# Kernel tuning notes

Hardware: AMD Instinct MI355X
Metric: run time of the kernel (lower is better)

## Reference

```python
import math
import jax, jax.numpy as jnp
import numpy as np

B, S, D, H, DH, R, V = 8, 1024, 1024, 8, 512, 36, 32002  # DH = d_model//2, HD = h*DH = 4096
HD = H * DH
LN_EPS = 1e-5


def setup_inputs() -> dict:
    key = jax.random.key(0)
    ks = jax.random.split(key, 16)

    def n(k, shp, std=0.02):
        return jax.random.normal(k, shp, jnp.float32) * std

    pre_words = jax.random.randint(ks[0], (B, S), 0, V)
    img_features = jax.random.normal(ks[1], (B, R, D), jnp.float32)
    exp_embed = n(ks[2], (V, D)).at[0].set(0.0)  # padding_idx=0
    # id2visual table: sparse nonneg rows over 36 regions; zero rows -> textual tokens
    id2vis = (jax.random.uniform(ks[3], (V, R)) < 0.05).astype(jnp.float32)
    # stacked params for 2 transformer layers; weights stored (in, out) so y = x @ W + b
    wq = n(ks[4], (2, D, HD)); bq = jnp.zeros((2, HD), jnp.float32)
    wk = n(ks[5], (2, D, HD)); bk = jnp.zeros((2, HD), jnp.float32)
    wv = n(ks[6], (2, D, HD)); bv = jnp.zeros((2, HD), jnp.float32)
    wo = n(ks[7], (2, HD, D)); bo = jnp.zeros((2, D), jnp.float32)
    w1 = n(ks[8], (2, D, D)); b1 = jnp.zeros((2, D), jnp.float32)
    w2 = n(ks[9], (2, D, D)); b2 = jnp.zeros((2, D), jnp.float32)
    ln1_g = jnp.ones((2, D), jnp.float32); ln1_b = jnp.zeros((2, D), jnp.float32)
    ln2_g = jnp.ones((2, D), jnp.float32); ln2_b = jnp.zeros((2, D), jnp.float32)
    return dict(pre_words=pre_words, img_features=img_features, exp_embed=exp_embed,
                id2vis=id2vis, wq=wq, bq=bq, wk=wk, bk=bk, wv=wv, bv=bv, wo=wo, bo=bo,
                w1=w1, b1=b1, w2=w2, b2=b2, ln1_g=ln1_g, ln1_b=ln1_b, ln2_g=ln2_g, ln2_b=ln2_b)


def _layer_norm(x, g, b):
    m = x.mean(-1, keepdims=True)
    v = ((x - m) ** 2).mean(-1, keepdims=True)
    return (x - m) / jnp.sqrt(v + LN_EPS) * g + b


def _softmax_one(x):
    # shifted-denominator softmax: exp(x - max) / (1 + sum exp(x - max))
    x = x - x.max(-1, keepdims=True)
    e = jnp.exp(x)
    return e / (1.0 + e.sum(-1, keepdims=True))


def reference(pre_words, img_features, exp_embed, id2vis, wq, bq, wk, bk, wv, bv,
              wo, bo, w1, b1, w2, b2, ln1_g, ln1_b, ln2_g, ln2_b):
    # token embedding: textual (masked to 0 where a visual row exists) + visual bmm
    te = exp_embed[pre_words]                       # (B,S,D)
    vids = id2vis[pre_words]                        # (B,S,R)
    word_mask = vids.sum(-1, keepdims=True) != 0    # (B,S,1)
    ve = jnp.einsum('bsr,brd->bsd', vids, img_features)
    x = jnp.where(word_mask, 0.0, te) + ve          # (B,S,D)

    scale = 1.0 / math.sqrt(DH)
    for i in range(2):  # two structurally identical transformer layers
        h = _layer_norm(x, ln1_g[i], ln1_b[i])
        q = (h @ wq[i] + bq[i]).reshape(B, S, H, DH).transpose(0, 2, 1, 3)
        k = (h @ wk[i] + bk[i]).reshape(B, S, H, DH).transpose(0, 2, 1, 3)
        v = (h @ wv[i] + bv[i]).reshape(B, S, H, DH).transpose(0, 2, 1, 3)
        attn = _softmax_one(jnp.einsum('bhqd,bhkd->bhqk', q, k) * scale)  # (B,H,S,S)
        o = jnp.einsum('bhqk,bhkd->bhqd', attn, v)
        o = o.transpose(0, 2, 1, 3).reshape(B, S, HD)
        x = x + (o @ wo[i] + bo[i])
        f = _layer_norm(x, ln2_g[i], ln2_b[i])
        f = jax.nn.gelu(f @ w1[i] + b1[i], approximate=False) @ w2[i] + b2[i]
        x = x + f
    return x
```

## Files before the change

### kernel.cpp

```cpp
#include <hip/hip_runtime.h>


using u16 = unsigned short;
typedef __attribute__((ext_vector_type(8))) short bf16x8;
typedef __attribute__((ext_vector_type(4))) float f32x4;

__device__ __forceinline__ float b2f(u16 u) {
  union { unsigned int i; float f; } v; v.i = ((unsigned int)u) << 16; return v.f;
}
__device__ __forceinline__ u16 f2b(float f) {
  union { float f; unsigned int i; } v; v.f = f;
  unsigned int i = v.i;
  return (u16)((i + 0x7FFFu + ((i >> 16) & 1u)) >> 16);
}
__device__ __forceinline__ float gelu_f(float x) {
  return 0.5f * x * (1.f + erff(x * 0.70710678118654752f));
}
__device__ __forceinline__ void async16(void* lds, const void* g) {
  __builtin_amdgcn_global_load_lds((const __attribute__((address_space(1))) void*)g,
                                   (__attribute__((address_space(3))) void*)lds, 16, 0, 0);
}
__device__ __forceinline__ void storeC(float* p, float v) { *p = v; }
__device__ __forceinline__ void storeC(u16* p, float v) { *p = f2b(v); }

__global__ __launch_bounds__(256) void embed_k(
    const int* __restrict__ words, const float* __restrict__ img,
    const float* __restrict__ emb, const float* __restrict__ id2v,
    float* __restrict__ x)
{
  __shared__ float vs[36];
  int tok = blockIdx.x, b = tok >> 10, t = threadIdx.x;
  int wd = words[tok];
  if (t < 36) vs[t] = id2v[(size_t)wd * 36 + t];
  __syncthreads();
  bool any = false;
#pragma unroll
  for (int r = 0; r < 36; ++r) any = any || (vs[r] != 0.f);
#pragma unroll
  for (int i = 0; i < 4; ++i) {
    int d = t + (i << 8);
    float acc = 0.f;
    for (int r = 0; r < 36; ++r) {
      float vv = vs[r];
      if (vv != 0.f) acc += vv * img[((size_t)(b * 36 + r) << 10) + d];
    }
    float te = any ? 0.f : emb[((size_t)wd << 10) + d];
    x[((size_t)tok << 10) + d] = te + acc;
  }
}

__global__ __launch_bounds__(256) void ln_k(
    const float* __restrict__ x, u16* __restrict__ out,
    const float* __restrict__ g, const float* __restrict__ bb)
{
  __shared__ float red[4];
  int row = blockIdx.x, t = threadIdx.x;
  const float* xr = x + ((size_t)row << 10);
  float v[4], s = 0.f;
#pragma unroll
  for (int i = 0; i < 4; ++i) { v[i] = xr[t + (i << 8)]; s += v[i]; }
#pragma unroll
  for (int o = 32; o; o >>= 1) s += __shfl_xor(s, o, 64);
  if ((t & 63) == 0) red[t >> 6] = s;
  __syncthreads();
  s = red[0] + red[1] + red[2] + red[3];
  float mean = s * 0.0009765625f;
  float q = 0.f;
#pragma unroll
  for (int i = 0; i < 4; ++i) { float d = v[i] - mean; q += d * d; }
  __syncthreads();
#pragma unroll
  for (int o = 32; o; o >>= 1) q += __shfl_xor(q, o, 64);
  if ((t & 63) == 0) red[t >> 6] = q;
  __syncthreads();
  q = red[0] + red[1] + red[2] + red[3];
  float rstd = rsqrtf(q * 0.0009765625f + 1e-5f);
  u16* orow = out + ((size_t)row << 10);
#pragma unroll
  for (int i = 0; i < 4; ++i) {
    int d = t + (i << 8);
    orow[d] = f2b((v[i] - mean) * rstd * g[d] + bb[d]);
  }
}

__global__ __launch_bounds__(256) void sm_k(const u16* __restrict__ S, u16* __restrict__ P)
{
  __shared__ float red[4];
  size_t row = blockIdx.x;
  int t = threadIdx.x;
  const u16* sr = S + (row << 10);
  ushort4 sv = *(const ushort4*)(sr + (t << 2));
  float v[4] = { b2f(sv.x), b2f(sv.y), b2f(sv.z), b2f(sv.w) };
  float m = fmaxf(fmaxf(v[0], v[1]), fmaxf(v[2], v[3]));
#pragma unroll
  for (int o = 32; o; o >>= 1) m = fmaxf(m, __shfl_xor(m, o, 64));
  if ((t & 63) == 0) red[t >> 6] = m;
  __syncthreads();
  m = fmaxf(fmaxf(red[0], red[1]), fmaxf(red[2], red[3]));
  float e[4], s = 0.f;
#pragma unroll
  for (int i = 0; i < 4; ++i) { e[i] = __expf(v[i] - m); s += e[i]; }
  __syncthreads();
#pragma unroll
  for (int o = 32; o; o >>= 1) s += __shfl_xor(s, o, 64);
  if ((t & 63) == 0) red[t >> 6] = s;
  __syncthreads();
  s = red[0] + red[1] + red[2] + red[3];
  float inv = 1.f / (1.f + s);
  ushort4 pv;
  pv.x = f2b(e[0] * inv); pv.y = f2b(e[1] * inv);
  pv.z = f2b(e[2] * inv); pv.w = f2b(e[3] * inv);
  *(ushort4*)(P + (row << 10) + (t << 2)) = pv;
}

__global__ __launch_bounds__(256) void tr_k(
    const float* __restrict__ src, u16* __restrict__ dst, int ls, int ld)
{
  __shared__ u16 tile[64][65];
  int c0 = blockIdx.x << 6, r0 = blockIdx.y << 6;
  int tx = threadIdx.x & 63, ty0 = threadIdx.x >> 6;
#pragma unroll
  for (int i = 0; i < 16; ++i) {
    int ty = (ty0 << 4) + i;
    tile[ty][tx] = f2b(src[(size_t)(r0 + ty) * ls + (c0 + tx)]);
  }
  __syncthreads();
#pragma unroll
  for (int i = 0; i < 16; ++i) {
    int ty = (ty0 << 4) + i;
    dst[(size_t)(c0 + ty) * ld + (r0 + tx)] = tile[tx][ty];
  }
}

template <typename CT, int ACT, int BIAS, int RESID>
__global__ __launch_bounds__(512, 1) void gemm8p(
    const u16* __restrict__ A, const u16* __restrict__ Bt,
    CT* __restrict__ C, const float* __restrict__ bias,
    const float* __restrict__ resid,
    int M, int N, int K, int lda, int ldb, int ldc, float scale,
    int zbase, int zdiv, int ga, int gb, int gc,
    long long aS1, long long aS2, long long bS1, long long bS2,
    long long cS1, long long cS2)
{
  __shared__ u16 lA[2][256 * 64];
  __shared__ u16 lB[2][256 * 64];
  const int nwg = gridDim.x * gridDim.y;
  const int id = blockIdx.y * gridDim.x + blockIdx.x;
  const int qq = nwg >> 3, rr8 = nwg & 7;
  const int xcd = id & 7, off = id >> 3;
  const int swz = (xcd < rr8 ? xcd * (qq + 1) : rr8 * (qq + 1) + (xcd - rr8) * qq) + off;
  const int bx = swz % gridDim.x, by = swz / gridDim.x;

  long long lz = blockIdx.z;
  long long gz = zbase + lz;
  long long zA = ga ? gz : lz, zB = gb ? gz : lz, zC = gc ? gz : lz;
  size_t aOff = (size_t)((zA / zdiv) * aS1 + (zA % zdiv) * aS2);
  size_t bOff = (size_t)((zB / zdiv) * bS1 + (zB % zdiv) * bS2);
  size_t cOff = (size_t)((zC / zdiv) * cS1 + (zC % zdiv) * cS2);
  const int m0 = by << 8, n0 = bx << 8;
  const int tid = threadIdx.x, lane = tid & 63, w = tid >> 6;
  const int wm = w >> 2, wn = w & 3;
  const int srow8 = lane >> 3;
  const int schunk = (lane & 7) ^ srow8;
  const int fr = lane & 15, hi = lane >> 4;

  f32x4 acc[8][4];
#pragma unroll
  for (int mi = 0; mi < 8; ++mi)
#pragma unroll
    for (int ni = 0; ni < 4; ++ni) acc[mi][ni] = 0.f;

  const u16* Ab = A + aOff;
  const u16* Bb = Bt + bOff;

  auto ST_B = [&](int buf, int k0) {
#pragma unroll
    for (int s = 0; s < 4; ++s) {
      const int rb = (s << 6) + (w << 3);
      async16(&lB[buf][rb << 6], Bb + (size_t)(n0 + rb + srow8) * ldb + (k0 + (schunk << 3)));
    }
  };
  auto ST_A02 = [&](int buf, int k0) {
#pragma unroll
    for (int s = 0; s < 4; s += 2) {
      const int rb = (s << 6) + (w << 3);
      async16(&lA[buf][rb << 6], Ab + (size_t)(m0 + rb + srow8) * lda + (k0 + (schunk << 3)));
    }
  };
  auto ST_A13 = [&](int buf, int k0) {
#pragma unroll
    for (int s = 1; s < 4; s += 2) {
      const int rb = (s << 6) + (w << 3);
      async16(&lA[buf][rb << 6], Ab + (size_t)(m0 + rb + srow8) * lda + (k0 + (schunk << 3)));
    }
  };

  const int nt = K >> 6;
  ST_B(0, 0); ST_A02(0, 0); ST_A13(0, 0);
  ST_B(1, 64); ST_A02(1, 64);

  for (int t = 0; t < nt; ++t) {
    const int cur = t & 1;
    if (t + 1 < nt) asm volatile("s_waitcnt vmcnt(6)" ::: "memory");
    else            asm volatile("s_waitcnt vmcnt(0)" ::: "memory");
    __builtin_amdgcn_s_barrier();
    __builtin_amdgcn_sched_barrier(0);

    bf16x8 b8[4][2];
    const int kt2 = (t + 2) << 6;
#pragma unroll
    for (int p = 0; p < 4; ++p) {
      if (p == 0) {
#pragma unroll
        for (int ni = 0; ni < 4; ++ni)
#pragma unroll
          for (int ks = 0; ks < 2; ++ks) {
            const int R = (wn << 6) + (ni << 4) + fr;
            const int q = (ks << 2) + hi;
            b8[ni][ks] = *(const bf16x8*)&lB[cur][(R << 6) + ((q ^ (R & 7)) << 3)];
          }
      }
      bf16x8 a8[2][2];
#pragma unroll
      for (int i = 0; i < 2; ++i)
#pragma unroll
        for (int ks = 0; ks < 2; ++ks) {
          const int mi = (p << 1) + i;
          const int R = (wm << 7) + (mi << 4) + fr;
          const int q = (ks << 2) + hi;
          a8[i][ks] = *(const bf16x8*)&lA[cur][(R << 6) + ((q ^ (R & 7)) << 3)];
        }
      if (p == 0) { if (t + 1 < nt) ST_A13(cur ^ 1, (t + 1) << 6); }
      else if (p == 1) { if (t + 2 < nt) ST_B(cur, kt2); }
      else if (p == 2) { if (t + 2 < nt) ST_A02(cur, kt2); }
      __builtin_amdgcn_s_barrier();
      asm volatile("s_waitcnt lgkmcnt(0)" ::: "memory");
      __builtin_amdgcn_sched_barrier(0);
      __builtin_amdgcn_s_setprio(1);
#pragma unroll
      for (int i = 0; i < 2; ++i)
#pragma unroll
        for (int ni = 0; ni < 4; ++ni)
#pragma unroll
          for (int ks = 0; ks < 2; ++ks)
            acc[(p << 1) + i][ni] =
                __builtin_amdgcn_mfma_f32_16x16x32_bf16(a8[i][ks], b8[ni][ks],
                                                        acc[(p << 1) + i][ni], 0, 0, 0);
      __builtin_amdgcn_s_setprio(0);
      __builtin_amdgcn_s_barrier();
      __builtin_amdgcn_sched_barrier(0);
    }
  }

  const int r4 = hi << 2, cc = fr;
#pragma unroll
  for (int mi = 0; mi < 8; ++mi) {
#pragma unroll
    for (int ni = 0; ni < 4; ++ni) {
      const int col = n0 + (wn << 6) + (ni << 4) + cc;
      float bcol = 0.f;
      if (BIAS == 1) bcol = bias[col];
#pragma unroll
      for (int j = 0; j < 4; ++j) {
        const int row = m0 + (wm << 7) + (mi << 4) + r4 + j;
        float v = acc[mi][ni][j] * scale + bcol;
        if (BIAS == 2) v += bias[row];
        if (ACT == 1) v = gelu_f(v);
        const size_t idx = cOff + (size_t)row * ldc + col;
        if (RESID) v += resid[idx];
        storeC(&C[idx], v);
      }
    }
  }
}

template <typename CT, int ACT, int BIAS, int RESID, int BN>
__global__ __launch_bounds__(256, 4) void gemm_t(
    const u16* __restrict__ A, const u16* __restrict__ Bt,
    CT* __restrict__ C, const float* __restrict__ bias,
    const float* __restrict__ resid,
    int M, int N, int K, int lda, int ldb, int ldc, float scale,
    int zbase, int zdiv, int ga, int gb, int gc,
    long long aS1, long long aS2, long long bS1, long long bS2,
    long long cS1, long long cS2)
{
  constexpr int NACC = BN / 32;
  __shared__ u16 lA[128 * 64];
  __shared__ u16 lB[BN * 64];
  const int nwg = gridDim.x * gridDim.y;
  const int id = blockIdx.y * gridDim.x + blockIdx.x;
  const int qq = nwg >> 3, rr8 = nwg & 7;
  const int xcd = id & 7, off = id >> 3;
  const int swz = (xcd < rr8 ? xcd * (qq + 1) : rr8 * (qq + 1) + (xcd - rr8) * qq) + off;
  const int bx = swz % gridDim.x, by = swz / gridDim.x;

  long long lz = blockIdx.z;
  long long gz = zbase + lz;
  long long zA = ga ? gz : lz, zB = gb ? gz : lz, zC = gc ? gz : lz;
  size_t aOff = (size_t)((zA / zdiv) * aS1 + (zA % zdiv) * aS2);
  size_t bOff = (size_t)((zB / zdiv) * bS1 + (zB % zdiv) * bS2);
  size_t cOff = (size_t)((zC / zdiv) * cS1 + (zC % zdiv) * cS2);
  const int m0 = by << 7, n0 = bx * BN;
  const int tid = threadIdx.x, lane = tid & 63, w = tid >> 6;
  const int wm = w >> 1, wn = w & 1;
  const int srow8 = lane >> 3;
  const int schunk = (lane & 7) ^ srow8;
  const int fr = lane & 15, hi = lane >> 4;

  f32x4 acc[4][NACC];
#pragma unroll
  for (int mi = 0; mi < 4; ++mi)
#pragma unroll
    for (int ni = 0; ni < NACC; ++ni) acc[mi][ni] = 0.f;

  const u16* Ab = A + aOff;
  const u16* Bb = Bt + bOff;

  for (int k0 = 0; k0 < K; k0 += 64) {
#pragma unroll
    for (int s = 0; s < 4; ++s) {
      const int rb = (s << 5) + (w << 3);
      async16(&lA[rb << 6], Ab + (size_t)(m0 + rb + srow8) * lda + (k0 + (schunk << 3)));
    }
#pragma unroll
    for (int s = 0; s < BN / 32; ++s) {
      const int rb = (s << 5) + (w << 3);
      async16(&lB[rb << 6], Bb + (size_t)(n0 + rb + srow8) * ldb + (k0 + (schunk << 3)));
    }
    __syncthreads();
#pragma unroll
    for (int ks = 0; ks < 2; ++ks) {
      const int q = (ks << 2) + hi;
      bf16x8 a8[4], b8[NACC];
#pragma unroll
      for (int mi = 0; mi < 4; ++mi) {
        const int R = (wm << 6) + (mi << 4) + fr;
        a8[mi] = *(const bf16x8*)&lA[(R << 6) + ((q ^ (R & 7)) << 3)];
      }
#pragma unroll
      for (int ni = 0; ni < NACC; ++ni) {
        const int R = wn * (BN / 2) + (ni << 4) + fr;
        b8[ni] = *(const bf16x8*)&lB[(R << 6) + ((q ^ (R & 7)) << 3)];
      }
#pragma unroll
      for (int mi = 0; mi < 4; ++mi)
#pragma unroll
        for (int ni = 0; ni < NACC; ++ni)
          acc[mi][ni] = __builtin_amdgcn_mfma_f32_16x16x32_bf16(a8[mi], b8[ni], acc[mi][ni], 0, 0, 0);
    }
    __syncthreads();
  }

  const int r4 = hi << 2, cc = fr;
#pragma unroll
  for (int mi = 0; mi < 4; ++mi) {
#pragma unroll
    for (int ni = 0; ni < NACC; ++ni) {
      const int col = n0 + wn * (BN / 2) + (ni << 4) + cc;
      float bcol = 0.f;
      if (BIAS == 1) bcol = bias[col];
#pragma unroll
      for (int j = 0; j < 4; ++j) {
        const int row = m0 + (wm << 6) + (mi << 4) + r4 + j;
        float v = acc[mi][ni][j] * scale + bcol;
        if (BIAS == 2) v += bias[row];
        if (ACT == 1) v = gelu_f(v);
        const size_t idx = cOff + (size_t)row * ldc + col;
        if (RESID) v += resid[idx];
        storeC(&C[idx], v);
      }
    }
  }
}

extern "C" void kernel_launch(void* const* d_in, const int* in_sizes, int n_in,
                              void* d_out, int out_size, void* d_ws, size_t ws_size,
                              hipStream_t stream)
{
  (void)in_sizes; (void)n_in; (void)out_size;
  const int*   pre_words = (const int*)d_in[0];
  const float* img  = (const float*)d_in[1];
  const float* emb  = (const float*)d_in[2];
  const float* id2v = (const float*)d_in[3];
  const float* wq = (const float*)d_in[4];  const float* bq = (const float*)d_in[5];
  const float* wk = (const float*)d_in[6];  const float* bk = (const float*)d_in[7];
  const float* wv = (const float*)d_in[8];  const float* bv = (const float*)d_in[9];
  const float* wo = (const float*)d_in[10]; const float* bo = (const float*)d_in[11];
  const float* w1 = (const float*)d_in[12]; const float* b1 = (const float*)d_in[13];
  const float* w2 = (const float*)d_in[14]; const float* b2 = (const float*)d_in[15];
  const float* ln1g = (const float*)d_in[16]; const float* ln1b = (const float*)d_in[17];
  const float* ln2g = (const float*)d_in[18]; const float* ln2b = (const float*)d_in[19];

  const size_t FIXED = 88080384 + (size_t)(1 << 16);
  int g = 1;
  for (int c = 8; c >= 1; c >>= 1)
    if (FIXED + (size_t)c * 33554432 + 4194304 <= ws_size) { g = c; break; }
  int nc = 1;
  int ncmax = 8 * g > 32 ? 32 : 8 * g;
  for (int c = ncmax; c >= 1; c >>= 1)
    if (FIXED + (size_t)g * 33554432 + (size_t)c * 4194304 <= ws_size) { nc = c; break; }

  char* p = (char*)d_ws;
  auto alloc = [&](size_t bytes) -> void* {
    void* r = (void*)p; p += (bytes + 255) & ~(size_t)255; return r;
  };
  float* x  = (float*)alloc((size_t)8192 * 1024 * 4);
  u16* h    = (u16*)alloc((size_t)8192 * 1024 * 2);
  u16* Qg   = (u16*)alloc((size_t)g * 1024 * 4096 * 2);
  u16* Og   = (u16*)alloc((size_t)g * 1024 * 4096 * 2);
  u16* ff   = Qg;
  u16* Kg   = (u16*)alloc((size_t)g * 1024 * 4096 * 2);
  u16* Vtg  = (u16*)alloc((size_t)g * 4096 * 1024 * 2);
  u16* wqt  = (u16*)alloc((size_t)4096 * 1024 * 2);
  u16* wkt  = (u16*)alloc((size_t)4096 * 1024 * 2);
  u16* wvt  = (u16*)alloc((size_t)4096 * 1024 * 2);
  u16* wot  = (u16*)alloc((size_t)1024 * 4096 * 2);
  u16* w1t  = (u16*)alloc((size_t)1024 * 1024 * 2);
  u16* w2t  = (u16*)alloc((size_t)1024 * 1024 * 2);
  u16* Sc   = (u16*)alloc((size_t)nc << 21);
  u16* Pp   = (u16*)alloc((size_t)nc << 21);

  embed_k<<<8192, 256, 0, stream>>>(pre_words, img, emb, id2v, x);

  const float qk_scale = 0.044194173824159216f;
  for (int L = 0; L < 2; ++L) {
    const float* WQ = wq + (size_t)L * 1024 * 4096;
    const float* WK = wk + (size_t)L * 1024 * 4096;
    const float* WV = wv + (size_t)L * 1024 * 4096;
    const float* WO = wo + (size_t)L * 4096 * 1024;
    const float* W1 = w1 + (size_t)L * 1024 * 1024;
    const float* W2 = w2 + (size_t)L * 1024 * 1024;

    tr_k<<<dim3(64, 16), 256, 0, stream>>>(WQ, wqt, 4096, 1024);
    tr_k<<<dim3(64, 16), 256, 0, stream>>>(WK, wkt, 4096, 1024);
    tr_k<<<dim3(64, 16), 256, 0, stream>>>(WV, wvt, 4096, 1024);
    tr_k<<<dim3(16, 64), 256, 0, stream>>>(WO, wot, 1024, 4096);
    tr_k<<<dim3(16, 16), 256, 0, stream>>>(W1, w1t, 1024, 1024);
    tr_k<<<dim3(16, 16), 256, 0, stream>>>(W2, w2t, 1024, 1024);

    ln_k<<<8192, 256, 0, stream>>>(x, h, ln1g + L * 1024, ln1b + L * 1024);

    for (int g0 = 0; g0 < 8; g0 += g) {
      const u16* hg = h + (size_t)g0 * 1048576;
      const int Mg = 1024 * g;
      gemm8p<u16, 0, 1, 0><<<dim3(16, Mg >> 8), 512, 0, stream>>>(
          hg, wqt, Qg, bq + (size_t)L * 4096, nullptr,
          Mg, 4096, 1024, 1024, 1024, 4096, 1.f,
          0, 1, 0, 0, 0, 0, 0, 0, 0, 0, 0);
      gemm8p<u16, 0, 1, 0><<<dim3(16, Mg >> 8), 512, 0, stream>>>(
          hg, wkt, Kg, bk + (size_t)L * 4096, nullptr,
          Mg, 4096, 1024, 1024, 1024, 4096, 1.f,
          0, 1, 0, 0, 0, 0, 0, 0, 0, 0, 0);
      gemm8p<u16, 0, 2, 0><<<dim3(4, 16, g), 512, 0, stream>>>(
          wvt, h, Vtg, bv + (size_t)L * 4096, nullptr,
          4096, 1024, 1024, 1024, 1024, 1024, 1.f,
          g0, 1, 0, 1, 0, 0, 0, 1048576LL, 0, 4194304LL, 0);
      for (int c0 = 0; c0 < 8 * g; c0 += nc) {
        gemm8p<u16, 0, 0, 0><<<dim3(4, 4, nc), 512, 0, stream>>>(
            Qg, Kg, Sc, nullptr, nullptr,
            1024, 1024, 512, 4096, 4096, 1024, qk_scale,
            c0, 8, 1, 1, 0,
            4194304LL, 512LL, 4194304LL, 512LL, 8388608LL, 1048576LL);
        sm_k<<<nc << 10, 256, 0, stream>>>(Sc, Pp);
        gemm8p<u16, 0, 0, 0><<<dim3(2, 4, nc), 512, 0, stream>>>(
            Pp, Vtg, Og, nullptr, nullptr,
            1024, 512, 1024, 1024, 1024, 4096, 1.f,
            c0, 8, 0, 1, 1,
            8388608LL, 1048576LL, 4194304LL, 524288LL, 4194304LL, 512LL);
      }
      gemm_t<float, 0, 1, 1, 64><<<dim3(16, Mg >> 7), 256, 0, stream>>>(
          Og, wot, x + (size_t)g0 * 1048576, bo + (size_t)L * 1024,
          x + (size_t)g0 * 1048576,
          Mg, 1024, 4096, 4096, 4096, 1024, 1.f,
          0, 1, 0, 0, 0, 0, 0, 0, 0, 0, 0);
    }

    ln_k<<<8192, 256, 0, stream>>>(x, h, ln2g + L * 1024, ln2b + L * 1024);

    gemm_t<u16, 1, 1, 0, 64><<<dim3(16, 64), 256, 0, stream>>>(
        h, w1t, ff, b1 + (size_t)L * 1024, nullptr,
        8192, 1024, 1024, 1024, 1024, 1024, 1.f,
        0, 1, 0, 0, 0, 0, 0, 0, 0, 0, 0);
    float* cdst = (L == 1) ? (float*)d_out : x;
    gemm_t<float, 0, 1, 1, 64><<<dim3(16, 64), 256, 0, stream>>>(
        ff, w2t, cdst, b2 + (size_t)L * 1024, x,
        8192, 1024, 1024, 1024, 1024, 1024, 1.f,
        0, 1, 0, 0, 0, 0, 0, 0, 0, 0, 0);
  }
}
```

Measured before the change: 1.497 ms.

## Fuse Q/K projection GEMMs, wave-per-row softmax, larger attention chunks

Result: no change. 1.500 ms (+0.2%).

```diff
diff --git a/kernel.cpp b/kernel.cpp
--- a/kernel.cpp
+++ b/kernel.cpp
@@ -85,32 +85,37 @@
 
 __global__ __launch_bounds__(256) void sm_k(const u16* __restrict__ S, u16* __restrict__ P)
 {
-  __shared__ float red[4];
-  size_t row = blockIdx.x;
-  int t = threadIdx.x;
-  const u16* sr = S + (row << 10);
-  ushort4 sv = *(const ushort4*)(sr + (t << 2));
-  float v[4] = { b2f(sv.x), b2f(sv.y), b2f(sv.z), b2f(sv.w) };
-  float m = fmaxf(fmaxf(v[0], v[1]), fmaxf(v[2], v[3]));
+  size_t row = ((size_t)blockIdx.x << 2) + (threadIdx.x >> 6);
+  const int lane = threadIdx.x & 63;
+  const u16* sr = S + (row << 10) + (lane << 4);
+  ushort4 sv[4];
+#pragma unroll
+  for (int i = 0; i < 4; ++i) sv[i] = *(const ushort4*)(sr + (i << 2));
+  float v[16];
+#pragma unroll
+  for (int i = 0; i < 4; ++i) {
+    v[4 * i + 0] = b2f(sv[i].x); v[4 * i + 1] = b2f(sv[i].y);
+    v[4 * i + 2] = b2f(sv[i].z); v[4 * i + 3] = b2f(sv[i].w);
+  }
+  float m = v[0];
+#pragma unroll
+  for (int i = 1; i < 16; ++i) m = fmaxf(m, v[i]);
 #pragma unroll
   for (int o = 32; o; o >>= 1) m = fmaxf(m, __shfl_xor(m, o, 64));
-  if ((t & 63) == 0) red[t >> 6] = m;
-  __syncthreads();
-  m = fmaxf(fmaxf(red[0], red[1]), fmaxf(red[2], red[3]));
-  float e[4], s = 0.f;
-#pragma unroll
-  for (int i = 0; i < 4; ++i) { e[i] = __expf(v[i] - m); s += e[i]; }
-  __syncthreads();
+  float s = 0.f;
+#pragma unroll
+  for (int i = 0; i < 16; ++i) { v[i] = __expf(v[i] - m); s += v[i]; }
 #pragma unroll
   for (int o = 32; o; o >>= 1) s += __shfl_xor(s, o, 64);
-  if ((t & 63) == 0) red[t >> 6] = s;
-  __syncthreads();
-  s = red[0] + red[1] + red[2] + red[3];
-  float inv = 1.f / (1.f + s);
-  ushort4 pv;
-  pv.x = f2b(e[0] * inv); pv.y = f2b(e[1] * inv);
-  pv.z = f2b(e[2] * inv); pv.w = f2b(e[3] * inv);
-  *(ushort4*)(P + (row << 10) + (t << 2)) = pv;
+  const float inv = 1.f / (1.f + s);
+  u16* pr = P + (row << 10) + (lane << 4);
+#pragma unroll
+  for (int i = 0; i < 4; ++i) {
+    ushort4 pv;
+    pv.x = f2b(v[4 * i + 0] * inv); pv.y = f2b(v[4 * i + 1] * inv);
+    pv.z = f2b(v[4 * i + 2] * inv); pv.w = f2b(v[4 * i + 3] * inv);
+    *(ushort4*)(pr + (i << 2)) = pv;
+  }
 }
 
 __global__ __launch_bounds__(256) void tr_k(
@@ -132,7 +137,7 @@
   }
 }
 
-template <typename CT, int ACT, int BIAS, int RESID>
+template <typename CT, int ACT, int BIAS, int RESID, int SPLIT>
 __global__ __launch_bounds__(512, 1) void gemm8p(
     const u16* __restrict__ A, const u16* __restrict__ Bt,
     CT* __restrict__ C, const float* __restrict__ bias,
@@ -140,7 +145,8 @@
     int M, int N, int K, int lda, int ldb, int ldc, float scale,
     int zbase, int zdiv, int ga, int gb, int gc,
     long long aS1, long long aS2, long long bS1, long long bS2,
-    long long cS1, long long cS2)
+    long long cS1, long long cS2,
+    const float* __restrict__ bias2, CT* __restrict__ C2)
 {
   __shared__ u16 lA[2][256 * 64];
   __shared__ u16 lB[2][256 * 64];
@@ -253,22 +259,27 @@
   }
 
   const int r4 = hi << 2, cc = fr;
+  const int half = N >> 1;
 #pragma unroll
   for (int mi = 0; mi < 8; ++mi) {
 #pragma unroll
     for (int ni = 0; ni < 4; ++ni) {
       const int col = n0 + (wn << 6) + (ni << 4) + cc;
+      CT* Cd = C;
+      int colx = col;
+      const float* bp = bias;
+      if (SPLIT && col >= half) { Cd = C2; colx = col - half; bp = bias2; }
       float bcol = 0.f;
-      if (BIAS == 1) bcol = bias[col];
+      if (BIAS == 1) bcol = bp[colx];
 #pragma unroll
       for (int j = 0; j < 4; ++j) {
         const int row = m0 + (wm << 7) + (mi << 4) + r4 + j;
         float v = acc[mi][ni][j] * scale + bcol;
         if (BIAS == 2) v += bias[row];
         if (ACT == 1) v = gelu_f(v);
-        const size_t idx = cOff + (size_t)row * ldc + col;
+        const size_t idx = cOff + (size_t)row * ldc + colx;
         if (RESID) v += resid[idx];
-        storeC(&C[idx], v);
+        storeC(&Cd[idx], v);
       }
     }
   }
@@ -396,7 +407,7 @@
   for (int c = 8; c >= 1; c >>= 1)
     if (FIXED + (size_t)c * 33554432 + 4194304 <= ws_size) { g = c; break; }
   int nc = 1;
-  int ncmax = 8 * g > 32 ? 32 : 8 * g;
+  int ncmax = 8 * g > 64 ? 64 : 8 * g;
   for (int c = ncmax; c >= 1; c >>= 1)
     if (FIXED + (size_t)g * 33554432 + (size_t)c * 4194304 <= ws_size) { nc = c; break; }
 
@@ -411,8 +422,7 @@
   u16* ff   = Qg;
   u16* Kg   = (u16*)alloc((size_t)g * 1024 * 4096 * 2);
   u16* Vtg  = (u16*)alloc((size_t)g * 4096 * 1024 * 2);
-  u16* wqt  = (u16*)alloc((size_t)4096 * 1024 * 2);
-  u16* wkt  = (u16*)alloc((size_t)4096 * 1024 * 2);
+  u16* wqkt = (u16*)alloc((size_t)8192 * 1024 * 2);
   u16* wvt  = (u16*)alloc((size_t)4096 * 1024 * 2);
   u16* wot  = (u16*)alloc((size_t)1024 * 4096 * 2);
   u16* w1t  = (u16*)alloc((size_t)1024 * 1024 * 2);
@@ -431,8 +441,8 @@
     const float* W1 = w1 + (size_t)L * 1024 * 1024;
     const float* W2 = w2 + (size_t)L * 1024 * 1024;
 
-    tr_k<<<dim3(64, 16), 256, 0, stream>>>(WQ, wqt, 4096, 1024);
-    tr_k<<<dim3(64, 16), 256, 0, stream>>>(WK, wkt, 4096, 1024);
+    tr_k<<<dim3(64, 16), 256, 0, stream>>>(WQ, wqkt, 4096, 1024);
+    tr_k<<<dim3(64, 16), 256, 0, stream>>>(WK, wqkt + (size_t)4096 * 1024, 4096, 1024);
     tr_k<<<dim3(64, 16), 256, 0, stream>>>(WV, wvt, 4096, 1024);
     tr_k<<<dim3(16, 64), 256, 0, stream>>>(WO, wot, 1024, 4096);
     tr_k<<<dim3(16, 16), 256, 0, stream>>>(W1, w1t, 1024, 1024);
@@ -443,30 +453,30 @@
     for (int g0 = 0; g0 < 8; g0 += g) {
       const u16* hg = h + (size_t)g0 * 1048576;
       const int Mg = 1024 * g;
-      gemm8p<u16, 0, 1, 0><<<dim3(16, Mg >> 8), 512, 0, stream>>>(
-          hg, wqt, Qg, bq + (size_t)L * 4096, nullptr,
-          Mg, 4096, 1024, 1024, 1024, 4096, 1.f,
-          0, 1, 0, 0, 0, 0, 0, 0, 0, 0, 0);
-      gemm8p<u16, 0, 1, 0><<<dim3(16, Mg >> 8), 512, 0, stream>>>(
-          hg, wkt, Kg, bk + (size_t)L * 4096, nullptr,
-          Mg, 4096, 1024, 1024, 1024, 4096, 1.f,
-          0, 1, 0, 0, 0, 0, 0, 0, 0, 0, 0);
-      gemm8p<u16, 0, 2, 0><<<dim3(4, 16, g), 512, 0, stream>>>(
+      gemm8p<u16, 0, 1, 0, 1><<<dim3(32, Mg >> 8), 512, 0, stream>>>(
+          hg, wqkt, Qg, bq + (size_t)L * 4096, nullptr,
+          Mg, 8192, 1024, 1024, 1024, 4096, 1.f,
+          0, 1, 0, 0, 0, 0, 0, 0, 0, 0, 0,
+          bk + (size_t)L * 4096, Kg);
+      gemm8p<u16, 0, 2, 0, 0><<<dim3(4, 16, g), 512, 0, stream>>>(
           wvt, h, Vtg, bv + (size_t)L * 4096, nullptr,
           4096, 1024, 1024, 1024, 1024, 1024, 1.f,
-          g0, 1, 0, 1, 0, 0, 0, 1048576LL, 0, 4194304LL, 0);
+          g0, 1, 0, 1, 0, 0, 0, 1048576LL, 0, 4194304LL, 0,
+          nullptr, nullptr);
       for (int c0 = 0; c0 < 8 * g; c0 += nc) {
-        gemm8p<u16, 0, 0, 0><<<dim3(4, 4, nc), 512, 0, stream>>>(
+        gemm8p<u16, 0, 0, 0, 0><<<dim3(4, 4, nc), 512, 0, stream>>>(
             Qg, Kg, Sc, nullptr, nullptr,
             1024, 1024, 512, 4096, 4096, 1024, qk_scale,
             c0, 8, 1, 1, 0,
-            4194304LL, 512LL, 4194304LL, 512LL, 8388608LL, 1048576LL);
-        sm_k<<<nc << 10, 256, 0, stream>>>(Sc, Pp);
-        gemm8p<u16, 0, 0, 0><<<dim3(2, 4, nc), 512, 0, stream>>>(
+            4194304LL, 512LL, 4194304LL, 512LL, 8388608LL, 1048576LL,
+            nullptr, nullptr);
+        sm_k<<<nc << 8, 256, 0, stream>>>(Sc, Pp);
+        gemm8p<u16, 0, 0, 0, 0><<<dim3(2, 4, nc), 512, 0, stream>>>(
             Pp, Vtg, Og, nullptr, nullptr,
             1024, 512, 1024, 1024, 1024, 4096, 1.f,
             c0, 8, 0, 1, 1,
-            8388608LL, 1048576LL, 4194304LL, 524288LL, 4194304LL, 512LL);
+            8388608LL, 1048576LL, 4194304LL, 524288LL, 4194304LL, 512LL,
+            nullptr, nullptr);
       }
       gemm_t<float, 0, 1, 1, 64><<<dim3(16, Mg >> 7), 256, 0, stream>>>(
           Og, wot, x + (size_t)g0 * 1048576, bo + (size_t)L * 1024,
```
